# Kernel tuning notes

Hardware: AMD Instinct MI355X
Metric: run time of the kernel (lower is better)

The kernel has to match this reference:

```python
import jax, jax.numpy as jnp
import numpy as np

B, T, I, H, F = 1024, 15, 256, 512, 8  # batch, seq(=BatchNorm1d(15)), input, hidden, out_features
G = 4 * H  # gate width, PyTorch gate order i,f,g,o


def setup_inputs() -> dict:
    key = jax.random.key(0)
    ks = jax.random.split(key, 10)
    s = lambda k, shape, sc=0.05: (jax.random.normal(k, shape, jnp.float32) * sc)
    return {
        "X": jax.random.normal(ks[0], (B, T, I), jnp.float32),
        # per-head stacked LSTM params (layer 0 and layer 1); bias = b_ih + b_hh combined
        "Wih0": s(ks[1], (F, G, I)), "Whh0": s(ks[2], (F, G, H)), "b0": s(ks[3], (F, G)),
        "Wih1": s(ks[4], (F, G, H)), "Whh1": s(ks[5], (F, G, H)), "b1": s(ks[6], (F, G)),
        # shared affine head: Linear(H,H) -> BatchNorm1d(15) -> ReLU -> Linear(H,1)
        "A1": s(ks[7], (H, H)), "c1": jnp.zeros((H,), jnp.float32),
        "gamma": jnp.ones((T,), jnp.float32), "beta": jnp.zeros((T,), jnp.float32),
        "A2": s(ks[8], (1, H)), "c2": jnp.zeros((1,), jnp.float32),
    }


def _lstm_layer(x, Wih, Whh, b):
    # x: [B,T,Din] -> [B,T,H]; PyTorch LSTM cell, gates ordered i,f,g,o
    xg = jnp.einsum('bti,gi->btg', x, Wih) + b  # precompute input projections [B,T,4H]
    Hh = Whh.shape[1]

    def step(carry, xg_t):
        h, c = carry
        g = xg_t + h @ Whh.T
        i_, f_, g_, o_ = jnp.split(g, 4, axis=-1)
        c = jax.nn.sigmoid(f_) * c + jax.nn.sigmoid(i_) * jnp.tanh(g_)
        h = jax.nn.sigmoid(o_) * jnp.tanh(c)
        return (h, c), h

    h0 = jnp.zeros((x.shape[0], Hh), x.dtype)
    _, hs = jax.lax.scan(step, (h0, h0), jnp.swapaxes(xg, 0, 1))
    return jnp.swapaxes(hs, 0, 1)  # [B,T,H]


def reference(X, Wih0, Whh0, b0, Wih1, Whh1, b1, A1, c1, gamma, beta, A2, c2):
    # F independent 2-layer LSTM stacks, vmapped over the head dim
    def per_head(wih0, whh0, bb0, wih1, whh1, bb1):
        y = _lstm_layer(X, wih0, whh0, bb0)
        return _lstm_layer(y, wih1, whh1, bb1)

    Y = jax.vmap(per_head)(Wih0, Whh0, b0, Wih1, Whh1, b1)  # [F,B,T,H]

    # shared affine head applied per head output (BN stats per head, training mode)
    h1 = jnp.einsum('fbth,oh->fbto', Y, A1) + c1            # [F,B,T,H]
    mean = h1.mean(axis=(1, 3), keepdims=True)              # per (head, channel=T)
    var = h1.var(axis=(1, 3), keepdims=True)                # biased var (torch BN train)
    hn = (h1 - mean) * jax.lax.rsqrt(var + 1e-5)
    hn = hn * gamma[None, None, :, None] + beta[None, None, :, None]
    out = jnp.einsum('fbth,oh->fbto', jax.nn.relu(hn), A2) + c2  # [F,B,T,1]
    return jnp.squeeze(out, -1).transpose(1, 2, 0)          # [B,T,F]
```

## Files before the change

kernel.cpp:

```cpp
#include <hip/hip_runtime.h>
#include <hip/hip_bf16.h>
#include <math.h>

#define Bb 1024
#define Tt 15
#define Ii 256
#define Hh 512
#define Ff 8
#define Gg 2048

typedef __attribute__((ext_vector_type(8))) short short8v;
typedef __attribute__((ext_vector_type(4))) float f32x4;

typedef const __attribute__((address_space(1))) void* gas_ptr;
typedef __attribute__((address_space(3))) void* las_ptr;

__device__ __forceinline__ float sigmoidf_(float x) {
    return __builtin_amdgcn_rcpf(1.0f + __expf(-x));
}
__device__ __forceinline__ float tanhf_(float x) {
    x = fminf(fmaxf(x, -15.0f), 15.0f);
    const float e = __expf(2.0f * x);
    return (e - 1.0f) * __builtin_amdgcn_rcpf(e + 1.0f);
}
__device__ __forceinline__ float bf2f(unsigned short u) {
    return __uint_as_float(((unsigned int)u) << 16);
}
__device__ __forceinline__ unsigned short f2bf(float f) {
    unsigned int u = __float_as_uint(f);
    u += 0x7fffu + ((u >> 16) & 1u);
    return (unsigned short)(u >> 16);
}

__global__ __launch_bounds__(256) void cvt_kernel(const float* __restrict__ in,
                                                  unsigned short* __restrict__ out, int n8) {
    const int i = blockIdx.x * 256 + threadIdx.x;
    if (i < n8) {
        const float4 v0 = ((const float4*)in)[i * 2];
        const float4 v1 = ((const float4*)in)[i * 2 + 1];
        union { unsigned short u[8]; short8v v; } ob;
        ob.u[0] = f2bf(v0.x); ob.u[1] = f2bf(v0.y); ob.u[2] = f2bf(v0.z); ob.u[3] = f2bf(v0.w);
        ob.u[4] = f2bf(v1.x); ob.u[5] = f2bf(v1.y); ob.u[6] = f2bf(v1.z); ob.u[7] = f2bf(v1.w);
        *(short8v*)&out[(size_t)i * 8] = ob.v;
    }
}

template<int MODE>
__device__ __forceinline__ void step_body(
    bool first, int f, int h0, int b0, int t, int hb, int bb,
    const short* ax, long axs, const short* ah, long ahs,
    const short* __restrict__ wxp, const short* __restrict__ whp,
    const float* __restrict__ bias, float* __restrict__ cbuf,
    unsigned short* __restrict__ ydst,
    float* __restrict__ part, char* smem)
{
    constexpr bool WG = (MODE != 2);
    constexpr int KX = (MODE == 0) ? Ii : Hh;
    constexpr int NX = KX / 64;
    const int NT = (MODE == 2) ? NX : (first ? NX : NX + Hh / 64);

    const int tid = threadIdx.x;
    const int wave = tid >> 6, lane = tid & 63;
    const int wm = (wave >> 1) * 64, wn = (wave & 1) * 64;

    short* sStage = (short*)smem;
    float* gt = (float*)smem;
    float* pr = (float*)(smem + 65536);

    f32x4 acc[4][4];
#pragma unroll
    for (int i = 0; i < 4; ++i)
#pragma unroll
        for (int j = 0; j < 4; ++j) acc[i][j] = (f32x4){0.f, 0.f, 0.f, 0.f};

    const int srow8 = lane >> 3;
    const int csrc  = (lane & 7) ^ srow8;
    const int frow  = lane & 15, fks = lane >> 4;

    auto stage = [&](int it, int buf) {
        const short* abase; long as; const short* wbase; int K; int kb;
        if (it < NX) { abase = ax; as = axs; wbase = wxp; K = KX; kb = it * 64; }
        else         { abase = ah; as = ahs; wbase = whp; K = Hh; kb = (it - NX) * 64; }
        short* dA = sStage + buf * 16384;
        short* dB = dA + 8192;
#pragma unroll
        for (int i = 0; i < 4; ++i) {
            const int inst = wave * 4 + i;
            const int row = inst * 8 + srow8;
            const short* srcA = abase + (size_t)row * as + kb + csrc * 8;
            __builtin_amdgcn_global_load_lds((gas_ptr)(const void*)srcA,
                (las_ptr)(void*)(dA + inst * 512), 16, 0, 0);
            const int wr = WG ? ((row >> 5) * Hh + h0 + (row & 31)) : (h0 + row);
            const short* srcB = wbase + (size_t)wr * K + kb + csrc * 8;
            __builtin_amdgcn_global_load_lds((gas_ptr)(const void*)srcB,
                (las_ptr)(void*)(dB + inst * 512), 16, 0, 0);
        }
    };

    auto compute = [&](int buf) {
        const short* bA = sStage + buf * 16384;
        const short* bB = bA + 8192;
        __builtin_amdgcn_s_setprio(1);
#pragma unroll
        for (int ks = 0; ks < 2; ++ks) {
            short8v av[4], bv[4];
#pragma unroll
            for (int i = 0; i < 4; ++i) {
                const int r = wm + i * 16 + frow;
                av[i] = *(const short8v*)&bA[r * 64 + (((fks + ks * 4) ^ (r & 7)) * 8)];
            }
#pragma unroll
            for (int j = 0; j < 4; ++j) {
                const int r = wn + j * 16 + frow;
                bv[j] = *(const short8v*)&bB[r * 64 + (((fks + ks * 4) ^ (r & 7)) * 8)];
            }
#pragma unroll
            for (int i = 0; i < 4; ++i)
#pragma unroll
                for (int j = 0; j < 4; ++j)
                    acc[i][j] = __builtin_amdgcn_mfma_f32_16x16x32_bf16(av[i], bv[j], acc[i][j], 0, 0, 0);
        }
        __builtin_amdgcn_s_setprio(0);
    };

    float bi[4] = {0.f, 0.f, 0.f, 0.f};
    if constexpr (MODE != 2) {
        const int hl = tid & 31;
#pragma unroll
        for (int g = 0; g < 4; ++g) bi[g] = bias[(size_t)f * Gg + g * Hh + h0 + hl];
        asm volatile("" : "+v"(bi[0]), "+v"(bi[1]), "+v"(bi[2]), "+v"(bi[3]));
    }

    stage(0, 0);
    for (int it = 0; it < NT; ++it) {
        if (it + 1 < NT) {
            stage(it + 1, (it + 1) & 1);
            asm volatile("s_waitcnt vmcnt(8)" ::: "memory");
        } else {
            asm volatile("s_waitcnt vmcnt(0)" ::: "memory");
        }
        __builtin_amdgcn_s_barrier();
        __builtin_amdgcn_sched_barrier(0);
        compute(it & 1);
        __builtin_amdgcn_sched_barrier(0);
        __builtin_amdgcn_s_barrier();
    }

    if constexpr (MODE != 2) {
        const int hl = tid & 31, bg = tid >> 5;
#pragma unroll
        for (int ch = 0; ch < 4; ++ch) {
            if ((wave >> 1) == (ch >> 1)) {
                const int i0 = (ch & 1) * 2;
#pragma unroll
                for (int i2 = 0; i2 < 2; ++i2) {
                    const int i = i0 + i2;
#pragma unroll
                    for (int j = 0; j < 4; ++j)
#pragma unroll
                        for (int r = 0; r < 4; ++r)
                            gt[(i2 * 16 + (lane >> 4) * 4 + r) * 132 + wn + j * 16 + (lane & 15)] = acc[i][j][r];
                }
            }
            __syncthreads();
#pragma unroll
            for (int ii = 0; ii < 4; ++ii) {
                const int rl = bg * 4 + ii;
                const int b = b0 + ch * 32 + rl;
                const float gi = gt[rl * 132 +      hl] + bi[0];
                const float gf = gt[rl * 132 + 32 + hl] + bi[1];
                const float gg = gt[rl * 132 + 64 + hl] + bi[2];
                const float go = gt[rl * 132 + 96 + hl] + bi[3];
                const size_t cidx = ((size_t)f * Bb + b) * Hh + h0 + hl;
                const float cold = first ? 0.f : cbuf[cidx];
                const float cn = sigmoidf_(gf) * cold + sigmoidf_(gi) * tanhf_(gg);
                const float hv = sigmoidf_(go) * tanhf_(cn);
                cbuf[cidx] = cn;
                const unsigned short hb2 = f2bf(hv);
                if (MODE == 0)
                    ydst[(((size_t)f * Bb + b) * Tt + t) * Hh + h0 + hl] = hb2;
                else
                    ydst[cidx] = hb2;
            }
            __syncthreads();
        }
    } else {
        const int rr2 = tid >> 3, cb = (tid & 7) * 16;
        float ssum = 0.f, ssq = 0.f;
#pragma unroll
        for (int ch = 0; ch < 4; ++ch) {
            if ((wave >> 1) == (ch >> 1)) {
                const int i0 = (ch & 1) * 2;
#pragma unroll
                for (int i2 = 0; i2 < 2; ++i2) {
                    const int i = i0 + i2;
#pragma unroll
                    for (int j = 0; j < 4; ++j)
#pragma unroll
                        for (int r = 0; r < 4; ++r)
                            gt[(i2 * 16 + (lane >> 4) * 4 + r) * 132 + wn + j * 16 + (lane & 15)] = acc[i][j][r];
                }
            }
            __syncthreads();
            const int b = b0 + ch * 32 + rr2;
            union { unsigned short u[8]; short8v v; } o1, o2;
#pragma unroll
            for (int u = 0; u < 8; ++u) {
                const unsigned short hb2 = f2bf(gt[rr2 * 132 + cb + u] + bias[h0 + cb + u]);
                const float hv = bf2f(hb2);
                ssum += hv; ssq += hv * hv;
                o1.u[u] = hb2;
            }
#pragma unroll
            for (int u = 0; u < 8; ++u) {
                const unsigned short hb2 = f2bf(gt[rr2 * 132 + cb + 8 + u] + bias[h0 + cb + 8 + u]);
                const float hv = bf2f(hb2);
                ssum += hv; ssq += hv * hv;
                o2.u[u] = hb2;
            }
            unsigned short* dst = ydst + (((size_t)f * Bb + b) * Tt + t) * Hh + h0 + cb;
            *(short8v*)dst = o1.v;
            *(short8v*)(dst + 8) = o2.v;
            __syncthreads();
        }
#pragma unroll
        for (int off2 = 32; off2 > 0; off2 >>= 1) {
            ssum += __shfl_down(ssum, off2);
            ssq  += __shfl_down(ssq,  off2);
        }
        if (lane == 0) { pr[wave * 2] = ssum; pr[wave * 2 + 1] = ssq; }
        __syncthreads();
        if (tid == 0) {
            float S = 0.f, Q = 0.f;
#pragma unroll
            for (int w = 0; w < 4; ++w) { S += pr[w * 2]; Q += pr[w * 2 + 1]; }
            const size_t pi = (((size_t)f * Tt + t) * 4 + hb) * 8 + bb;
            part[pi * 2] = S; part[pi * 2 + 1] = Q;
        }
    }
}

__global__ __launch_bounds__(256) void step_merged(
    const short* __restrict__ Xbf, short* __restrict__ ybuf,
    short* __restrict__ h1A, short* __restrict__ h1B,
    const short* __restrict__ W0x, const short* __restrict__ W0h,
    const short* __restrict__ W1x, const short* __restrict__ W1h,
    const short* __restrict__ A1bf,
    const float* __restrict__ b0p, const float* __restrict__ b1p,
    const float* __restrict__ c1v,
    float* __restrict__ c0buf, float* __restrict__ c1buf,
    float* __restrict__ part, int d)
{
    __shared__ __align__(16) char smem[65600];
    const int f = blockIdx.x;
    const int zz = blockIdx.z;

    if (zz < 8) {
        const int t = d;
        if (t >= Tt) return;
        const int hb = blockIdx.y, h0 = hb * 32, b0 = zz * 128;
        const bool first = (t == 0);
        const short* ax = Xbf + ((size_t)b0 * Tt + t) * Ii;
        const short* ah = first ? nullptr
                                : ybuf + (((size_t)f * Bb + b0) * Tt + (t - 1)) * Hh;
        step_body<0>(first, f, h0, b0, t, hb, zz,
                     ax, (long)Tt * Ii, ah, (long)Tt * Hh,
                     W0x + (size_t)f * Gg * Ii, W0h + (size_t)f * Gg * Hh,
                     b0p, c0buf, (unsigned short*)ybuf, part, smem);
    } else if (zz < 16) {
        const int t = d - 1;
        if (t < 0 || t >= Tt) return;
        const int bb = zz - 8;
        const int hb = blockIdx.y, h0 = hb * 32, b0 = bb * 128;
        const bool first = (t == 0);
        short* hn = (t & 1) ? h1A : h1B;
        const short* hp = (t & 1) ? h1B : h1A;
        const short* ax = ybuf + (((size_t)f * Bb + b0) * Tt + t) * Hh;
        const short* ah = first ? nullptr : hp + ((size_t)f * Bb + b0) * Hh;
        step_body<1>(first, f, h0, b0, t, hb, bb,
                     ax, (long)Tt * Hh, ah, (long)Hh,
                     W1x + (size_t)f * Gg * Hh, W1h + (size_t)f * Gg * Hh,
                     b1p, c1buf, (unsigned short*)hn, part, smem);
    } else {
        const int t = d - 2;
        if (t < 0) return;
        const int hb = blockIdx.y & 3, h0 = hb * 128;
        const int bb = (zz - 16) * 4 + (blockIdx.y >> 2), b0 = bb * 128;
        const short* hn = (t & 1) ? h1A : h1B;
        const short* ax = hn + ((size_t)f * Bb + b0) * Hh;
        step_body<2>(false, f, h0, b0, t, hb, bb,
                     ax, (long)Hh, nullptr, 0L,
                     A1bf, nullptr,
                     c1v, nullptr, (unsigned short*)ybuf, part, smem);
    }
}

__global__ void stats_combine_kernel(const float* __restrict__ part, float* __restrict__ stats)
{
    const int i = threadIdx.x;
    if (i < Ff * Tt) {
        float s = 0.f, q = 0.f;
        for (int j = 0; j < 32; ++j) { s += part[(i * 32 + j) * 2]; q += part[(i * 32 + j) * 2 + 1]; }
        const float n = (float)((size_t)Bb * Hh);
        const float mean = s / n;
        const float var  = q / n - mean * mean;
        stats[i * 2]     = mean;
        stats[i * 2 + 1] = rsqrtf(var + 1e-5f);
    }
}

__global__ __launch_bounds__(256) void out_kernel(
    const unsigned short* __restrict__ htmp, const float* __restrict__ stats,
    const float* __restrict__ gamma, const float* __restrict__ beta,
    const float* __restrict__ A2, const float* __restrict__ c2,
    float* __restrict__ out)
{
    const int wave = threadIdx.x >> 6;
    const int lane = threadIdx.x & 63;
    const size_t row = (size_t)blockIdx.x * 4 + wave;
    const int t = (int)(row % Tt);
    const size_t fb = row / Tt;
    const int b = (int)(fb % Bb);
    const int f = (int)(fb / Bb);

    const float mean = stats[(f * Tt + t) * 2];
    const float inv  = stats[(f * Tt + t) * 2 + 1];
    const float ga = gamma[t], be = beta[t];
    const unsigned short* hrow = htmp + row * Hh;

    union { float4 f4; unsigned short u[8]; } hv;
    hv.f4 = *(const float4*)(hrow + lane * 8);
    const float4 a0 = *(const float4*)(A2 + lane * 8);
    const float4 a1 = *(const float4*)(A2 + lane * 8 + 4);
    const float a2v[8] = {a0.x, a0.y, a0.z, a0.w, a1.x, a1.y, a1.z, a1.w};

    float acc = 0.f;
#pragma unroll
    for (int j = 0; j < 8; ++j) {
        const float x = (bf2f(hv.u[j]) - mean) * inv * ga + be;
        acc += fmaxf(x, 0.f) * a2v[j];
    }
#pragma unroll
    for (int off = 32; off > 0; off >>= 1) acc += __shfl_down(acc, off);
    if (lane == 0) out[(size_t)b * Tt * Ff + (size_t)t * Ff + f] = acc + c2[0];
}

extern "C" void kernel_launch(void* const* d_in, const int* in_sizes, int n_in,
                              void* d_out, int out_size, void* d_ws, size_t ws_size,
                              hipStream_t stream) {
    const float* X     = (const float*)d_in[0];
    const float* Wih0  = (const float*)d_in[1];
    const float* Whh0  = (const float*)d_in[2];
    const float* b0p   = (const float*)d_in[3];
    const float* Wih1  = (const float*)d_in[4];
    const float* Whh1  = (const float*)d_in[5];
    const float* b1p   = (const float*)d_in[6];
    const float* A1    = (const float*)d_in[7];
    const float* c1v   = (const float*)d_in[8];
    const float* gamma = (const float*)d_in[9];
    const float* beta  = (const float*)d_in[10];
    const float* A2    = (const float*)d_in[11];
    const float* c2    = (const float*)d_in[12];
    float* out = (float*)d_out;

    char* ws = (char*)d_ws;
    size_t off = 0;
    short* Xbf    = (short*)(ws + off); off += (size_t)Bb * Tt * Ii * 2;
    short* Wih0bf = (short*)(ws + off); off += (size_t)Ff * Gg * Ii * 2;
    short* Whh0bf = (short*)(ws + off); off += (size_t)Ff * Gg * Hh * 2;
    short* Wih1bf = (short*)(ws + off); off += (size_t)Ff * Gg * Hh * 2;
    short* Whh1bf = (short*)(ws + off); off += (size_t)Ff * Gg * Hh * 2;
    short* A1bf   = (short*)(ws + off); off += (size_t)Hh * Hh * 2;
    short* ybuf   = (short*)(ws + off); off += (size_t)Ff * Bb * Tt * Hh * 2;
    short* h1A    = (short*)(ws + off); off += (size_t)Ff * Bb * Hh * 2;
    short* h1B    = (short*)(ws + off); off += (size_t)Ff * Bb * Hh * 2;
    float* c0buf  = (float*)(ws + off); off += (size_t)Ff * Bb * Hh * 4;
    float* c1buf  = (float*)(ws + off); off += (size_t)Ff * Bb * Hh * 4;
    float* part   = (float*)(ws + off); off += (size_t)Ff * Tt * 32 * 2 * 4;
    float* stats  = (float*)(ws + off); off += (size_t)Ff * Tt * 2 * 4;

    const dim3 blk(256);
    cvt_kernel<<<dim3((Bb * Tt * Ii / 8 + 255) / 256), blk, 0, stream>>>(X, (unsigned short*)Xbf, Bb * Tt * Ii / 8);
    cvt_kernel<<<dim3((Ff * Gg * Ii / 8 + 255) / 256), blk, 0, stream>>>(Wih0, (unsigned short*)Wih0bf, Ff * Gg * Ii / 8);
    cvt_kernel<<<dim3((Ff * Gg * Hh / 8 + 255) / 256), blk, 0, stream>>>(Whh0, (unsigned short*)Whh0bf, Ff * Gg * Hh / 8);
    cvt_kernel<<<dim3((Ff * Gg * Hh / 8 + 255) / 256), blk, 0, stream>>>(Wih1, (unsigned short*)Wih1bf, Ff * Gg * Hh / 8);
    cvt_kernel<<<dim3((Ff * Gg * Hh / 8 + 255) / 256), blk, 0, stream>>>(Whh1, (unsigned short*)Whh1bf, Ff * Gg * Hh / 8);
    cvt_kernel<<<dim3((Hh * Hh / 8 + 255) / 256), blk, 0, stream>>>(A1, (unsigned short*)A1bf, Hh * Hh / 8);

    const dim3 gmerged(Ff, 16, 18);
    for (int d = 0; d <= Tt + 1; ++d) {
        step_merged<<<gmerged, blk, 0, stream>>>(
            Xbf, ybuf, h1A, h1B,
            Wih0bf, Whh0bf, Wih1bf, Whh1bf, A1bf,
            b0p, b1p, c1v, c0buf, c1buf, part, d);
    }

    stats_combine_kernel<<<dim3(1), dim3(128), 0, stream>>>(part, stats);
    out_kernel<<<dim3(Ff * Bb * Tt / 4), blk, 0, stream>>>((const unsigned short*)ybuf, stats,
        gamma, beta, A2, c2, out);
    (void)in_sizes; (void)n_in; (void)out_size; (void)ws_size;
}
```

Measured before the change: 1.439 ms.

## Widen LSTM step tiles to 128x256 with 512-thread blocks and bf16 cell state

Each block now covers 128 batch rows by 256 gate columns (64 hidden units per gate) using 8 waves and 512 threads, up from 128x128 with 4 waves. This halves the grid along the hidden dimension, so activation rows are staged and reused across more weight columns per block. The cell-state buffers also move from fp32 to bf16 to halve their read and write traffic. Costs: more LDS per block (about 96KB), possibly fewer resident blocks, and extra rounding error because the cell state is stored at reduced precision across timesteps.

```diff
diff --git a/kernel.cpp b/kernel.cpp
--- a/kernel.cpp
+++ b/kernel.cpp
@@ -50,7 +50,7 @@
     bool first, int f, int h0, int b0, int t, int hb, int bb,
     const short* ax, long axs, const short* ah, long ahs,
     const short* __restrict__ wxp, const short* __restrict__ whp,
-    const float* __restrict__ bias, float* __restrict__ cbuf,
+    const float* __restrict__ bias, unsigned short* __restrict__ cbuf,
     unsigned short* __restrict__ ydst,
     float* __restrict__ part, char* smem)
 {
@@ -61,11 +61,11 @@
 
     const int tid = threadIdx.x;
     const int wave = tid >> 6, lane = tid & 63;
-    const int wm = (wave >> 1) * 64, wn = (wave & 1) * 64;
+    const int wm = (wave >> 2) * 64, wn = (wave & 3) * 64;
 
     short* sStage = (short*)smem;
     float* gt = (float*)smem;
-    float* pr = (float*)(smem + 65536);
+    float* pr = (float*)(smem + 98304);
 
     f32x4 acc[4][4];
 #pragma unroll
@@ -81,24 +81,29 @@
         const short* abase; long as; const short* wbase; int K; int kb;
         if (it < NX) { abase = ax; as = axs; wbase = wxp; K = KX; kb = it * 64; }
         else         { abase = ah; as = ahs; wbase = whp; K = Hh; kb = (it - NX) * 64; }
-        short* dA = sStage + buf * 16384;
+        short* dA = sStage + buf * 24576;
         short* dB = dA + 8192;
 #pragma unroll
-        for (int i = 0; i < 4; ++i) {
-            const int inst = wave * 4 + i;
-            const int row = inst * 8 + srow8;
-            const short* srcA = abase + (size_t)row * as + kb + csrc * 8;
-            __builtin_amdgcn_global_load_lds((gas_ptr)(const void*)srcA,
-                (las_ptr)(void*)(dA + inst * 512), 16, 0, 0);
-            const int wr = WG ? ((row >> 5) * Hh + h0 + (row & 31)) : (h0 + row);
-            const short* srcB = wbase + (size_t)wr * K + kb + csrc * 8;
-            __builtin_amdgcn_global_load_lds((gas_ptr)(const void*)srcB,
-                (las_ptr)(void*)(dB + inst * 512), 16, 0, 0);
+        for (int i = 0; i < 6; ++i) {
+            const int q = wave * 6 + i;
+            if (q < 16) {
+                const int row = q * 8 + srow8;
+                const short* srcA = abase + (size_t)row * as + kb + csrc * 8;
+                __builtin_amdgcn_global_load_lds((gas_ptr)(const void*)srcA,
+                    (las_ptr)(void*)(dA + q * 512), 16, 0, 0);
+            } else {
+                const int qb = q - 16;
+                const int row = qb * 8 + srow8;
+                const int wr = WG ? ((row >> 6) * Hh + h0 + (row & 63)) : (h0 + row);
+                const short* srcB = wbase + (size_t)wr * K + kb + csrc * 8;
+                __builtin_amdgcn_global_load_lds((gas_ptr)(const void*)srcB,
+                    (las_ptr)(void*)(dB + qb * 512), 16, 0, 0);
+            }
         }
     };
 
     auto compute = [&](int buf) {
-        const short* bA = sStage + buf * 16384;
+        const short* bA = sStage + buf * 24576;
         const short* bB = bA + 8192;
         __builtin_amdgcn_s_setprio(1);
 #pragma unroll
@@ -125,7 +130,7 @@
 
     float bi[4] = {0.f, 0.f, 0.f, 0.f};
     if constexpr (MODE != 2) {
-        const int hl = tid & 31;
+        const int hl = tid & 63;
 #pragma unroll
         for (int g = 0; g < 4; ++g) bi[g] = bias[(size_t)f * Gg + g * Hh + h0 + hl];
         asm volatile("" : "+v"(bi[0]), "+v"(bi[1]), "+v"(bi[2]), "+v"(bi[3]));
@@ -135,7 +140,7 @@
     for (int it = 0; it < NT; ++it) {
         if (it + 1 < NT) {
             stage(it + 1, (it + 1) & 1);
-            asm volatile("s_waitcnt vmcnt(8)" ::: "memory");
+            asm volatile("s_waitcnt vmcnt(6)" ::: "memory");
         } else {
             asm volatile("s_waitcnt vmcnt(0)" ::: "memory");
         }
@@ -147,10 +152,10 @@
     }
 
     if constexpr (MODE != 2) {
-        const int hl = tid & 31, bg = tid >> 5;
+        const int hl = tid & 63, rg = tid >> 6;
 #pragma unroll
         for (int ch = 0; ch < 4; ++ch) {
-            if ((wave >> 1) == (ch >> 1)) {
+            if ((wave >> 2) == (ch >> 1)) {
                 const int i0 = (ch & 1) * 2;
 #pragma unroll
                 for (int i2 = 0; i2 < 2; ++i2) {
@@ -159,23 +164,23 @@
                     for (int j = 0; j < 4; ++j)
 #pragma unroll
                         for (int r = 0; r < 4; ++r)
-                            gt[(i2 * 16 + (lane >> 4) * 4 + r) * 132 + wn + j * 16 + (lane & 15)] = acc[i][j][r];
+                            gt[(i2 * 16 + (lane >> 4) * 4 + r) * 260 + wn + j * 16 + (lane & 15)] = acc[i][j][r];
                 }
             }
             __syncthreads();
 #pragma unroll
             for (int ii = 0; ii < 4; ++ii) {
-                const int rl = bg * 4 + ii;
+                const int rl = rg * 4 + ii;
                 const int b = b0 + ch * 32 + rl;
-                const float gi = gt[rl * 132 +      hl] + bi[0];
-                const float gf = gt[rl * 132 + 32 + hl] + bi[1];
-                const float gg = gt[rl * 132 + 64 + hl] + bi[2];
-                const float go = gt[rl * 132 + 96 + hl] + bi[3];
+                const float gi = gt[rl * 260 +       hl] + bi[0];
+                const float gf = gt[rl * 260 +  64 + hl] + bi[1];
+                const float gg = gt[rl * 260 + 128 + hl] + bi[2];
+                const float go = gt[rl * 260 + 192 + hl] + bi[3];
                 const size_t cidx = ((size_t)f * Bb + b) * Hh + h0 + hl;
-                const float cold = first ? 0.f : cbuf[cidx];
+                const float cold = first ? 0.f : bf2f(cbuf[cidx]);
                 const float cn = sigmoidf_(gf) * cold + sigmoidf_(gi) * tanhf_(gg);
                 const float hv = sigmoidf_(go) * tanhf_(cn);
-                cbuf[cidx] = cn;
+                cbuf[cidx] = f2bf(cn);
                 const unsigned short hb2 = f2bf(hv);
                 if (MODE == 0)
                     ydst[(((size_t)f * Bb + b) * Tt + t) * Hh + h0 + hl] = hb2;
@@ -185,11 +190,11 @@
             __syncthreads();
         }
     } else {
-        const int rr2 = tid >> 3, cb = (tid & 7) * 16;
+        const int rr2 = tid >> 4, cb = (tid & 15) * 16;
         float ssum = 0.f, ssq = 0.f;
 #pragma unroll
         for (int ch = 0; ch < 4; ++ch) {
-            if ((wave >> 1) == (ch >> 1)) {
+            if ((wave >> 2) == (ch >> 1)) {
                 const int i0 = (ch & 1) * 2;
 #pragma unroll
                 for (int i2 = 0; i2 < 2; ++i2) {
@@ -198,7 +203,7 @@
                     for (int j = 0; j < 4; ++j)
 #pragma unroll
                         for (int r = 0; r < 4; ++r)
-                            gt[(i2 * 16 + (lane >> 4) * 4 + r) * 132 + wn + j * 16 + (lane & 15)] = acc[i][j][r];
+                            gt[(i2 * 16 + (lane >> 4) * 4 + r) * 260 + wn + j * 16 + (lane & 15)] = acc[i][j][r];
                 }
             }
             __syncthreads();
@@ -206,14 +211,14 @@
             union { unsigned short u[8]; short8v v; } o1, o2;
 #pragma unroll
             for (int u = 0; u < 8; ++u) {
-                const unsigned short hb2 = f2bf(gt[rr2 * 132 + cb + u] + bias[h0 + cb + u]);
+                const unsigned short hb2 = f2bf(gt[rr2 * 260 + cb + u] + bias[h0 + cb + u]);
                 const float hv = bf2f(hb2);
                 ssum += hv; ssq += hv * hv;
                 o1.u[u] = hb2;
             }
 #pragma unroll
             for (int u = 0; u < 8; ++u) {
-                const unsigned short hb2 = f2bf(gt[rr2 * 132 + cb + 8 + u] + bias[h0 + cb + 8 + u]);
+                const unsigned short hb2 = f2bf(gt[rr2 * 260 + cb + 8 + u] + bias[h0 + cb + 8 + u]);
                 const float hv = bf2f(hb2);
                 ssum += hv; ssq += hv * hv;
                 o2.u[u] = hb2;
@@ -233,14 +238,14 @@
         if (tid == 0) {
             float S = 0.f, Q = 0.f;
 #pragma unroll
-            for (int w = 0; w < 4; ++w) { S += pr[w * 2]; Q += pr[w * 2 + 1]; }
-            const size_t pi = (((size_t)f * Tt + t) * 4 + hb) * 8 + bb;
+            for (int w = 0; w < 8; ++w) { S += pr[w * 2]; Q += pr[w * 2 + 1]; }
+            const size_t pi = (((size_t)f * Tt + t) * 2 + hb) * 8 + bb;
             part[pi * 2] = S; part[pi * 2 + 1] = Q;
         }
     }
 }
 
-__global__ __launch_bounds__(256) void step_merged(
+__global__ __launch_bounds__(512) void step_merged(
     const short* __restrict__ Xbf, short* __restrict__ ybuf,
     short* __restrict__ h1A, short* __restrict__ h1B,
     const short* __restrict__ W0x, const short* __restrict__ W0h,
@@ -248,22 +253,22 @@
     const short* __restrict__ A1bf,
     const float* __restrict__ b0p, const float* __restrict__ b1p,
     const float* __restrict__ c1v,
-    float* __restrict__ c0buf, float* __restrict__ c1buf,
+    unsigned short* __restrict__ c0buf, unsigned short* __restrict__ c1buf,
     float* __restrict__ part, int d)
 {
-    __shared__ __align__(16) char smem[65600];
+    __shared__ __align__(16) char smem[98304 + 64];
     const int f = blockIdx.x;
     const int zz = blockIdx.z;
 
     if (zz < 8) {
         const int t = d;
         if (t >= Tt) return;
-        const int hb = blockIdx.y, h0 = hb * 32, b0 = zz * 128;
+        const int h0 = blockIdx.y * 64, b0 = zz * 128;
         const bool first = (t == 0);
         const short* ax = Xbf + ((size_t)b0 * Tt + t) * Ii;
         const short* ah = first ? nullptr
                                 : ybuf + (((size_t)f * Bb + b0) * Tt + (t - 1)) * Hh;
-        step_body<0>(first, f, h0, b0, t, hb, zz,
+        step_body<0>(first, f, h0, b0, t, 0, zz,
                      ax, (long)Tt * Ii, ah, (long)Tt * Hh,
                      W0x + (size_t)f * Gg * Ii, W0h + (size_t)f * Gg * Hh,
                      b0p, c0buf, (unsigned short*)ybuf, part, smem);
@@ -271,21 +276,21 @@
         const int t = d - 1;
         if (t < 0 || t >= Tt) return;
         const int bb = zz - 8;
-        const int hb = blockIdx.y, h0 = hb * 32, b0 = bb * 128;
+        const int h0 = blockIdx.y * 64, b0 = bb * 128;
         const bool first = (t == 0);
         short* hn = (t & 1) ? h1A : h1B;
         const short* hp = (t & 1) ? h1B : h1A;
         const short* ax = ybuf + (((size_t)f * Bb + b0) * Tt + t) * Hh;
         const short* ah = first ? nullptr : hp + ((size_t)f * Bb + b0) * Hh;
-        step_body<1>(first, f, h0, b0, t, hb, bb,
+        step_body<1>(first, f, h0, b0, t, 0, bb,
                      ax, (long)Tt * Hh, ah, (long)Hh,
                      W1x + (size_t)f * Gg * Hh, W1h + (size_t)f * Gg * Hh,
                      b1p, c1buf, (unsigned short*)hn, part, smem);
     } else {
         const int t = d - 2;
         if (t < 0) return;
-        const int hb = blockIdx.y & 3, h0 = hb * 128;
-        const int bb = (zz - 16) * 4 + (blockIdx.y >> 2), b0 = bb * 128;
+        const int hb = zz - 16, h0 = hb * 256;
+        const int bb = blockIdx.y, b0 = bb * 128;
         const short* hn = (t & 1) ? h1A : h1B;
         const short* ax = hn + ((size_t)f * Bb + b0) * Hh;
         step_body<2>(false, f, h0, b0, t, hb, bb,
@@ -300,7 +305,7 @@
     const int i = threadIdx.x;
     if (i < Ff * Tt) {
         float s = 0.f, q = 0.f;
-        for (int j = 0; j < 32; ++j) { s += part[(i * 32 + j) * 2]; q += part[(i * 32 + j) * 2 + 1]; }
+        for (int j = 0; j < 16; ++j) { s += part[(i * 16 + j) * 2]; q += part[(i * 16 + j) * 2 + 1]; }
         const float n = (float)((size_t)Bb * Hh);
         const float mean = s / n;
         const float var  = q / n - mean * mean;
@@ -374,9 +379,9 @@
     short* ybuf   = (short*)(ws + off); off += (size_t)Ff * Bb * Tt * Hh * 2;
     short* h1A    = (short*)(ws + off); off += (size_t)Ff * Bb * Hh * 2;
     short* h1B    = (short*)(ws + off); off += (size_t)Ff * Bb * Hh * 2;
-    float* c0buf  = (float*)(ws + off); off += (size_t)Ff * Bb * Hh * 4;
-    float* c1buf  = (float*)(ws + off); off += (size_t)Ff * Bb * Hh * 4;
-    float* part   = (float*)(ws + off); off += (size_t)Ff * Tt * 32 * 2 * 4;
+    unsigned short* c0buf = (unsigned short*)(ws + off); off += (size_t)Ff * Bb * Hh * 2;
+    unsigned short* c1buf = (unsigned short*)(ws + off); off += (size_t)Ff * Bb * Hh * 2;
+    float* part   = (float*)(ws + off); off += (size_t)Ff * Tt * 16 * 2 * 4;
     float* stats  = (float*)(ws + off); off += (size_t)Ff * Tt * 2 * 4;
 
     const dim3 blk(256);
@@ -387,9 +392,10 @@
     cvt_kernel<<<dim3((Ff * Gg * Hh / 8 + 255) / 256), blk, 0, stream>>>(Whh1, (unsigned short*)Whh1bf, Ff * Gg * Hh / 8);
     cvt_kernel<<<dim3((Hh * Hh / 8 + 255) / 256), blk, 0, stream>>>(A1, (unsigned short*)A1bf, Hh * Hh / 8);
 
-    const dim3 gmerged(Ff, 16, 18);
+    const dim3 gmerged(Ff, 8, 18);
+    const dim3 blk512(512);
     for (int d = 0; d <= Tt + 1; ++d) {
-        step_merged<<<gmerged, blk, 0, stream>>>(
+        step_merged<<<gmerged, blk512, 0, stream>>>(
             Xbf, ybuf, h1A, h1B,
             Wih0bf, Whh0bf, Wih1bf, Whh1bf, A1bf,
             b0p, b1p, c1v, c0buf, c1buf, part, d);
```

New measurement: 1.670 ms. 1.16x slower.

## Permute LSTM weight rows so gate epilogue runs directly from MFMA registers

Applied to the files above, without the earlier changes.

Weights are converted to bf16 with a permuted row order, so each wave's MFMA output columns hold the i,f,g,o gates for the same hidden unit. The LSTM cell update and the affine-head epilogue then read accumulators directly instead of round-tripping through shared memory with several __syncthreads per chunk. This removes LDS traffic and block barriers in the epilogue. The cost is scattered 2-byte global stores and a more complex weight-conversion kernel.

```diff
diff --git a/kernel.cpp b/kernel.cpp
--- a/kernel.cpp
+++ b/kernel.cpp
@@ -45,6 +45,27 @@
     }
 }
 
+__global__ __launch_bounds__(256) void cvt_wperm_kernel(const float* __restrict__ in,
+                                                        unsigned short* __restrict__ out,
+                                                        int Kc, int nchunks) {
+    const int i = blockIdx.x * 256 + threadIdx.x;
+    if (i < nchunks) {
+        const int k8 = i % Kc;
+        const int r  = (i / Kc) & 127;
+        const int hb = (i / (Kc * 128)) & 15;
+        const int f  = i / (Kc * 128 * 16);
+        const int gate = (r >> 4) & 3;
+        const int hl = (r & 15) + ((r >> 6) << 4);
+        const size_t src = ((size_t)f * Gg + gate * Hh + hb * 32 + hl) * (size_t)(Kc * 8) + k8 * 8;
+        const float4 v0 = *(const float4*)(in + src);
+        const float4 v1 = *(const float4*)(in + src + 4);
+        union { unsigned short u[8]; short8v v; } ob;
+        ob.u[0] = f2bf(v0.x); ob.u[1] = f2bf(v0.y); ob.u[2] = f2bf(v0.z); ob.u[3] = f2bf(v0.w);
+        ob.u[4] = f2bf(v1.x); ob.u[5] = f2bf(v1.y); ob.u[6] = f2bf(v1.z); ob.u[7] = f2bf(v1.w);
+        *(short8v*)&out[(size_t)i * 8] = ob.v;
+    }
+}
+
 template<int MODE>
 __device__ __forceinline__ void step_body(
     bool first, int f, int h0, int b0, int t, int hb, int bb,
@@ -54,7 +75,6 @@
     unsigned short* __restrict__ ydst,
     float* __restrict__ part, char* smem)
 {
-    constexpr bool WG = (MODE != 2);
     constexpr int KX = (MODE == 0) ? Ii : Hh;
     constexpr int NX = KX / 64;
     const int NT = (MODE == 2) ? NX : (first ? NX : NX + Hh / 64);
@@ -64,7 +84,6 @@
     const int wm = (wave >> 1) * 64, wn = (wave & 1) * 64;
 
     short* sStage = (short*)smem;
-    float* gt = (float*)smem;
     float* pr = (float*)(smem + 65536);
 
     f32x4 acc[4][4];
@@ -90,8 +109,7 @@
             const short* srcA = abase + (size_t)row * as + kb + csrc * 8;
             __builtin_amdgcn_global_load_lds((gas_ptr)(const void*)srcA,
                 (las_ptr)(void*)(dA + inst * 512), 16, 0, 0);
-            const int wr = WG ? ((row >> 5) * Hh + h0 + (row & 31)) : (h0 + row);
-            const short* srcB = wbase + (size_t)wr * K + kb + csrc * 8;
+            const short* srcB = wbase + (size_t)row * K + kb + csrc * 8;
             __builtin_amdgcn_global_load_lds((gas_ptr)(const void*)srcB,
                 (las_ptr)(void*)(dB + inst * 512), 16, 0, 0);
         }
@@ -123,13 +141,16 @@
         __builtin_amdgcn_s_setprio(0);
     };
 
+    const int hoff = ((wn >> 6) << 4) + (lane & 15);
     float bi[4] = {0.f, 0.f, 0.f, 0.f};
     if constexpr (MODE != 2) {
-        const int hl = tid & 31;
-#pragma unroll
-        for (int g = 0; g < 4; ++g) bi[g] = bias[(size_t)f * Gg + g * Hh + h0 + hl];
-        asm volatile("" : "+v"(bi[0]), "+v"(bi[1]), "+v"(bi[2]), "+v"(bi[3]));
-    }
+#pragma unroll
+        for (int g = 0; g < 4; ++g) bi[g] = bias[(size_t)f * Gg + g * Hh + h0 + hoff];
+    } else {
+#pragma unroll
+        for (int j = 0; j < 4; ++j) bi[j] = bias[h0 + wn + j * 16 + (lane & 15)];
+    }
+    asm volatile("" : "+v"(bi[0]), "+v"(bi[1]), "+v"(bi[2]), "+v"(bi[3]));
 
     stage(0, 0);
     for (int it = 0; it < NT; ++it) {
@@ -147,82 +168,43 @@
     }
 
     if constexpr (MODE != 2) {
-        const int hl = tid & 31, bg = tid >> 5;
-#pragma unroll
-        for (int ch = 0; ch < 4; ++ch) {
-            if ((wave >> 1) == (ch >> 1)) {
-                const int i0 = (ch & 1) * 2;
-#pragma unroll
-                for (int i2 = 0; i2 < 2; ++i2) {
-                    const int i = i0 + i2;
-#pragma unroll
-                    for (int j = 0; j < 4; ++j)
-#pragma unroll
-                        for (int r = 0; r < 4; ++r)
-                            gt[(i2 * 16 + (lane >> 4) * 4 + r) * 132 + wn + j * 16 + (lane & 15)] = acc[i][j][r];
-                }
-            }
-            __syncthreads();
-#pragma unroll
-            for (int ii = 0; ii < 4; ++ii) {
-                const int rl = bg * 4 + ii;
-                const int b = b0 + ch * 32 + rl;
-                const float gi = gt[rl * 132 +      hl] + bi[0];
-                const float gf = gt[rl * 132 + 32 + hl] + bi[1];
-                const float gg = gt[rl * 132 + 64 + hl] + bi[2];
-                const float go = gt[rl * 132 + 96 + hl] + bi[3];
-                const size_t cidx = ((size_t)f * Bb + b) * Hh + h0 + hl;
+#pragma unroll
+        for (int i = 0; i < 4; ++i)
+#pragma unroll
+            for (int r = 0; r < 4; ++r) {
+                const int b = b0 + wm + i * 16 + ((lane >> 4) << 2) + r;
+                const float gi = acc[i][0][r] + bi[0];
+                const float gf = acc[i][1][r] + bi[1];
+                const float gg = acc[i][2][r] + bi[2];
+                const float go = acc[i][3][r] + bi[3];
+                const size_t cidx = ((size_t)f * Bb + b) * Hh + h0 + hoff;
                 const float cold = first ? 0.f : cbuf[cidx];
                 const float cn = sigmoidf_(gf) * cold + sigmoidf_(gi) * tanhf_(gg);
                 const float hv = sigmoidf_(go) * tanhf_(cn);
                 cbuf[cidx] = cn;
                 const unsigned short hb2 = f2bf(hv);
                 if (MODE == 0)
-                    ydst[(((size_t)f * Bb + b) * Tt + t) * Hh + h0 + hl] = hb2;
+                    ydst[(((size_t)f * Bb + b) * Tt + t) * Hh + h0 + hoff] = hb2;
                 else
                     ydst[cidx] = hb2;
             }
-            __syncthreads();
-        }
     } else {
-        const int rr2 = tid >> 3, cb = (tid & 7) * 16;
         float ssum = 0.f, ssq = 0.f;
 #pragma unroll
-        for (int ch = 0; ch < 4; ++ch) {
-            if ((wave >> 1) == (ch >> 1)) {
-                const int i0 = (ch & 1) * 2;
-#pragma unroll
-                for (int i2 = 0; i2 < 2; ++i2) {
-                    const int i = i0 + i2;
-#pragma unroll
-                    for (int j = 0; j < 4; ++j)
-#pragma unroll
-                        for (int r = 0; r < 4; ++r)
-                            gt[(i2 * 16 + (lane >> 4) * 4 + r) * 132 + wn + j * 16 + (lane & 15)] = acc[i][j][r];
+        for (int i = 0; i < 4; ++i)
+#pragma unroll
+            for (int r = 0; r < 4; ++r) {
+                const int b = b0 + wm + i * 16 + ((lane >> 4) << 2) + r;
+                unsigned short* dst = ydst + (((size_t)f * Bb + b) * Tt + t) * Hh;
+#pragma unroll
+                for (int j = 0; j < 4; ++j) {
+                    const int o = h0 + wn + j * 16 + (lane & 15);
+                    const unsigned short hb2 = f2bf(acc[i][j][r] + bi[j]);
+                    const float hv = bf2f(hb2);
+                    ssum += hv; ssq += hv * hv;
+                    dst[o] = hb2;
                 }
             }
-            __syncthreads();
-            const int b = b0 + ch * 32 + rr2;
-            union { unsigned short u[8]; short8v v; } o1, o2;
-#pragma unroll
-            for (int u = 0; u < 8; ++u) {
-                const unsigned short hb2 = f2bf(gt[rr2 * 132 + cb + u] + bias[h0 + cb + u]);
-                const float hv = bf2f(hb2);
-                ssum += hv; ssq += hv * hv;
-                o1.u[u] = hb2;
-            }
-#pragma unroll
-            for (int u = 0; u < 8; ++u) {
-                const unsigned short hb2 = f2bf(gt[rr2 * 132 + cb + 8 + u] + bias[h0 + cb + 8 + u]);
-                const float hv = bf2f(hb2);
-                ssum += hv; ssq += hv * hv;
-                o2.u[u] = hb2;
-            }
-            unsigned short* dst = ydst + (((size_t)f * Bb + b) * Tt + t) * Hh + h0 + cb;
-            *(short8v*)dst = o1.v;
-            *(short8v*)(dst + 8) = o2.v;
-            __syncthreads();
-        }
 #pragma unroll
         for (int off2 = 32; off2 > 0; off2 >>= 1) {
             ssum += __shfl_down(ssum, off2);
@@ -265,7 +247,8 @@
                                 : ybuf + (((size_t)f * Bb + b0) * Tt + (t - 1)) * Hh;
         step_body<0>(first, f, h0, b0, t, hb, zz,
                      ax, (long)Tt * Ii, ah, (long)Tt * Hh,
-                     W0x + (size_t)f * Gg * Ii, W0h + (size_t)f * Gg * Hh,
+                     W0x + ((size_t)f * 16 + hb) * 128 * Ii,
+                     W0h + ((size_t)f * 16 + hb) * 128 * Hh,
                      b0p, c0buf, (unsigned short*)ybuf, part, smem);
     } else if (zz < 16) {
         const int t = d - 1;
@@ -279,7 +262,8 @@
         const short* ah = first ? nullptr : hp + ((size_t)f * Bb + b0) * Hh;
         step_body<1>(first, f, h0, b0, t, hb, bb,
                      ax, (long)Tt * Hh, ah, (long)Hh,
-                     W1x + (size_t)f * Gg * Hh, W1h + (size_t)f * Gg * Hh,
+                     W1x + ((size_t)f * 16 + hb) * 128 * Hh,
+                     W1h + ((size_t)f * 16 + hb) * 128 * Hh,
                      b1p, c1buf, (unsigned short*)hn, part, smem);
     } else {
         const int t = d - 2;
@@ -290,7 +274,7 @@
         const short* ax = hn + ((size_t)f * Bb + b0) * Hh;
         step_body<2>(false, f, h0, b0, t, hb, bb,
                      ax, (long)Hh, nullptr, 0L,
-                     A1bf, nullptr,
+                     A1bf + (size_t)h0 * Hh, nullptr,
                      c1v, nullptr, (unsigned short*)ybuf, part, smem);
     }
 }
@@ -381,10 +365,14 @@
 
     const dim3 blk(256);
     cvt_kernel<<<dim3((Bb * Tt * Ii / 8 + 255) / 256), blk, 0, stream>>>(X, (unsigned short*)Xbf, Bb * Tt * Ii / 8);
-    cvt_kernel<<<dim3((Ff * Gg * Ii / 8 + 255) / 256), blk, 0, stream>>>(Wih0, (unsigned short*)Wih0bf, Ff * Gg * Ii / 8);
-    cvt_kernel<<<dim3((Ff * Gg * Hh / 8 + 255) / 256), blk, 0, stream>>>(Whh0, (unsigned short*)Whh0bf, Ff * Gg * Hh / 8);
-    cvt_kernel<<<dim3((Ff * Gg * Hh / 8 + 255) / 256), blk, 0, stream>>>(Wih1, (unsigned short*)Wih1bf, Ff * Gg * Hh / 8);
-    cvt_kernel<<<dim3((Ff * Gg * Hh / 8 + 255) / 256), blk, 0, stream>>>(Whh1, (unsigned short*)Whh1bf, Ff * Gg * Hh / 8);
+    cvt_wperm_kernel<<<dim3((Ff * Gg * Ii / 8 + 255) / 256), blk, 0, stream>>>(
+        Wih0, (unsigned short*)Wih0bf, Ii / 8, Ff * Gg * Ii / 8);
+    cvt_wperm_kernel<<<dim3((Ff * Gg * Hh / 8 + 255) / 256), blk, 0, stream>>>(
+        Whh0, (unsigned short*)Whh0bf, Hh / 8, Ff * Gg * Hh / 8);
+    cvt_wperm_kernel<<<dim3((Ff * Gg * Hh / 8 + 255) / 256), blk, 0, stream>>>(
+        Wih1, (unsigned short*)Wih1bf, Hh / 8, Ff * Gg * Hh / 8);
+    cvt_wperm_kernel<<<dim3((Ff * Gg * Hh / 8 + 255) / 256), blk, 0, stream>>>(
+        Whh1, (unsigned short*)Whh1bf, Hh / 8, Ff * Gg * Hh / 8);
     cvt_kernel<<<dim3((Hh * Hh / 8 + 255) / 256), blk, 0, stream>>>(A1, (unsigned short*)A1bf, Hh * Hh / 8);
 
     const dim3 gmerged(Ff, 16, 18);
```

Result: faster. 1.382 ms (-3.9%).
